# Kernel optimization log

Measured on AMD Instinct MI355X. Metric: run time of the kernel, lower is better.

The kernel has to match this reference:

```python
import jax, jax.numpy as jnp
import numpy as np

EPS = 1e-5

def layernorm(x, g, b):
    mu = jnp.mean(x, axis=-1, keepdims=True)
    var = jnp.mean((x - mu) ** 2, axis=-1, keepdims=True)
    return (x - mu) * jax.lax.rsqrt(var + EPS) * g + b

def cswin_attn(q, k, v, lepe_w, lepe_b, H, W, H_sp, W_sp, num_heads):
    # q,k,v: (B, L, C) with C = branch dim
    B, L, C = q.shape
    d = C // num_heads
    nH, nW = H // H_sp, W // W_sp
    def to_win(t):
        t = t.transpose(0, 2, 1).reshape(B, C, nH, H_sp, nW, W_sp)
        t = t.transpose(0, 2, 4, 3, 5, 1).reshape(B * nH * nW, H_sp * W_sp, num_heads, d)
        return t.transpose(0, 2, 1, 3)  # (Bw, h, N, d)
    kw = to_win(k)
    vw = to_win(v)
    # q windows as images for LePE depthwise conv
    qi = q.transpose(0, 2, 1).reshape(B, C, nH, H_sp, nW, W_sp)
    qi = qi.transpose(0, 2, 4, 1, 3, 5).reshape(B * nH * nW, C, H_sp, W_sp)
    lepe = jax.lax.conv_general_dilated(qi, lepe_w, (1, 1), 'SAME',
                                        feature_group_count=C,
                                        dimension_numbers=('NCHW', 'OIHW', 'NCHW'))
    lepe = lepe + lepe_b[None, :, None, None]
    lepe = lepe.reshape(-1, num_heads, d, H_sp * W_sp).transpose(0, 1, 3, 2)
    qw = qi.reshape(-1, num_heads, d, H_sp * W_sp).transpose(0, 1, 3, 2) * (float(d) ** -0.5)
    attn = jax.nn.softmax(jnp.einsum('whnd,whmd->whnm', qw, kw), axis=-1)
    out = jnp.einsum('whnm,whmd->whnd', attn, vw) + lepe  # (Bw, h, N, d)
    out = out.transpose(0, 2, 1, 3).reshape(B, nH, nW, H_sp, W_sp, C)
    out = out.transpose(0, 1, 3, 2, 4, 5).reshape(B, H * W, C)
    return out

def setup_inputs() -> dict:
    key = jax.random.key(0)
    ks = jax.random.split(key, 20)
    B, C, H, W = 8, 128, 64, 64
    ch_z = 512
    hid = 4 * C
    Cb = C // 2  # branch dim
    s = lambda fin: (1.0 / np.sqrt(fin))
    inp = {
        'x': jax.random.normal(ks[0], (B, C, H, W), jnp.float32),
        'z': jax.random.normal(ks[1], (B, ch_z), jnp.float32),
        'ln1_g': jnp.ones((C,), jnp.float32), 'ln1_b': jnp.zeros((C,), jnp.float32),
        'ln2_g': jnp.ones((C,), jnp.float32), 'ln2_b': jnp.zeros((C,), jnp.float32),
        'Wz1': jax.random.normal(ks[2], (C, ch_z), jnp.float32) * s(ch_z),
        'Wz2': jax.random.normal(ks[3], (C, ch_z), jnp.float32) * s(ch_z),
        'Wqkv': jax.random.normal(ks[4], (3 * C, C), jnp.float32) * s(C),
        'Wproj': jax.random.normal(ks[5], (C, C), jnp.float32) * s(C),
        'bproj': jnp.zeros((C,), jnp.float32),
        'lepe_w0': jax.random.normal(ks[6], (Cb, 1, 3, 3), jnp.float32) * (1.0 / 3.0),
        'lepe_b0': jnp.zeros((Cb,), jnp.float32),
        'lepe_w1': jax.random.normal(ks[7], (Cb, 1, 3, 3), jnp.float32) * (1.0 / 3.0),
        'lepe_b1': jnp.zeros((Cb,), jnp.float32),
        'W1': jax.random.normal(ks[8], (hid, C), jnp.float32) * s(C),
        'b1': jnp.zeros((hid,), jnp.float32),
        'W2': jax.random.normal(ks[9], (C, hid), jnp.float32) * s(hid),
        'b2': jnp.zeros((C,), jnp.float32),
    }
    return inp

def reference(x, z, ln1_g, ln1_b, ln2_g, ln2_b, Wz1, Wz2, Wqkv, Wproj, bproj,
              lepe_w0, lepe_b0, lepe_w1, lepe_b1, W1, b1, W2, b2):
    B, C, H, W = x.shape
    nh = 4  # num_heads // 2 per branch
    ss = 8  # split_size
    Cb = C // 2
    xf = x.reshape(B, C, H * W).transpose(0, 2, 1)  # (B, L, C)
    # code-conditioned attention branch
    z1 = z @ Wz1.T  # (B, C)
    h1 = layernorm(xf, ln1_g, ln1_b) + z1[:, None, :]
    qkv = (h1 @ Wqkv.T).reshape(B, H * W, 3, C).transpose(2, 0, 1, 3)  # (3, B, L, C)
    q, k, v = qkv[0], qkv[1], qkv[2]
    x1 = cswin_attn(q[..., :Cb], k[..., :Cb], v[..., :Cb], lepe_w0, lepe_b0, H, W, H, ss, nh)
    x2 = cswin_attn(q[..., Cb:], k[..., Cb:], v[..., Cb:], lepe_w1, lepe_b1, H, W, ss, W, nh)
    att = jnp.concatenate([x1, x2], axis=2) @ Wproj.T + bproj
    xf = xf + att
    # code-conditioned MLP branch
    z2 = z @ Wz2.T
    h2 = layernorm(xf, ln2_g, ln2_b) + z2[:, None, :]
    mlp = jax.nn.gelu(h2 @ W1.T + b1, approximate=False) @ W2.T + b2
    xf = xf + mlp
    return xf.transpose(0, 2, 1).reshape(B, C, H, W)
```

## Files before the change

kernel.cpp:

```cpp
#include <hip/hip_runtime.h>
#include <cstddef>

__device__ __forceinline__ float b2f(unsigned short u) {
  return __uint_as_float(((unsigned int)u) << 16);
}
__device__ __forceinline__ unsigned short f2b(float f) {
  unsigned int u = __float_as_uint(f);
  u = u + 0x7FFFu + ((u >> 16) & 1u);
  return (unsigned short)(u >> 16);
}
__device__ __forceinline__ unsigned int pk2(float lo, float hi) {
  unsigned int ulo = __float_as_uint(lo) + 0x8000u;
  unsigned int uhi = __float_as_uint(hi) + 0x8000u;
  return __builtin_amdgcn_perm(uhi, ulo, 0x07060302u);
}
__device__ __forceinline__ float gelu_exact(float x) {
  return 0.5f * x * (1.0f + erff(x * 0.70710678118654752f));
}

#if defined(__has_builtin)
#if __has_builtin(__builtin_amdgcn_exp2f)
#define EXP2(x) __builtin_amdgcn_exp2f(x)
#else
#define EXP2(x) __expf((x) * 0.6931471805599453f)
#endif
#else
#define EXP2(x) __expf((x) * 0.6931471805599453f)
#endif

typedef __attribute__((ext_vector_type(8))) short bf16x8;
typedef __attribute__((ext_vector_type(4))) float f32x4;

__global__ void k_detect(const unsigned short* __restrict__ g,
                         unsigned int* __restrict__ flag) {
  if (threadIdx.x == 0 && blockIdx.x == 0) *flag = (g[0] == 0x3F80u) ? 1u : 0u;
}

struct Ptrs18 { const void* p[18]; };
__constant__ const int c_off[19] = {
    0, 4096, 4224, 4352, 4480, 4608, 70144, 135680, 184832, 201216,
    201344, 201920, 201984, 202560, 202624, 268160, 268672, 334208, 334336};

__global__ __launch_bounds__(256) void k_convert(Ptrs18 ptrs,
                                                 const unsigned int* __restrict__ flagp,
                                                 unsigned short* __restrict__ dst) {
  int idx = blockIdx.x * 256 + threadIdx.x;
  if (idx >= 334336) return;
  unsigned int flag = *flagp;
  int i = 0;
#pragma unroll
  for (int t = 1; t < 18; ++t) i += (idx >= c_off[t]);
  int local = idx - c_off[i];
  if (flag) dst[idx] = ((const unsigned short*)ptrs.p[i])[local];
  else      dst[idx] = f2b(((const float*)ptrs.p[i])[local]);
}

__global__ __launch_bounds__(256) void k_transpose_in(const void* __restrict__ x,
                                                      const unsigned int* __restrict__ flagp,
                                                      float* __restrict__ xf) {
  __shared__ float t[32][33];
  unsigned int flag = *flagp;
  int b = blockIdx.z;
  int l0 = blockIdx.x * 32, c0 = blockIdx.y * 32;
  int tx = threadIdx.x & 31, ty = threadIdx.x >> 5;
#pragma unroll
  for (int i = 0; i < 32; i += 8) {
    size_t gi = ((size_t)b * 128 + c0 + ty + i) * 4096 + l0 + tx;
    t[ty + i][tx] = flag ? b2f(((const unsigned short*)x)[gi]) : ((const float*)x)[gi];
  }
  __syncthreads();
#pragma unroll
  for (int i = 0; i < 32; i += 8)
    xf[((size_t)b * 4096 + l0 + ty + i) * 128 + c0 + tx] = t[tx][ty + i];
}

__global__ __launch_bounds__(256) void k_transpose_out(const float* __restrict__ xf,
                                                       const unsigned int* __restrict__ flagp,
                                                       void* __restrict__ out) {
  __shared__ float t[32][33];
  unsigned int flag = *flagp;
  int b = blockIdx.z;
  int l0 = blockIdx.x * 32, c0 = blockIdx.y * 32;
  int tx = threadIdx.x & 31, ty = threadIdx.x >> 5;
#pragma unroll
  for (int i = 0; i < 32; i += 8)
    t[ty + i][tx] = xf[((size_t)b * 4096 + l0 + ty + i) * 128 + c0 + tx];
  __syncthreads();
#pragma unroll
  for (int i = 0; i < 32; i += 8) {
    size_t gi = ((size_t)b * 128 + c0 + ty + i) * 4096 + l0 + tx;
    float v = t[tx][ty + i];
    if (flag) ((unsigned short*)out)[gi] = f2b(v);
    else      ((float*)out)[gi] = v;
  }
}

__global__ __launch_bounds__(256) void k_zmm(const unsigned short* __restrict__ z,
                                             const unsigned short* __restrict__ Wz1,
                                             const unsigned short* __restrict__ Wz2,
                                             float* __restrict__ zz) {
  __shared__ float sz[512];
  int b = blockIdx.x, tid = threadIdx.x;
  sz[tid]       = b2f(z[b * 512 + tid]);
  sz[tid + 256] = b2f(z[b * 512 + 256 + tid]);
  __syncthreads();
  const unsigned short* W = (tid < 128) ? Wz1 : Wz2;
  int c = tid & 127;
  const unsigned short* wr = W + c * 512;
  float acc = 0.f;
  for (int k = 0; k < 512; k += 4) {
    ushort4 wv = *(const ushort4*)&wr[k];
    acc += b2f(wv.x) * sz[k] + b2f(wv.y) * sz[k + 1] + b2f(wv.z) * sz[k + 2] + b2f(wv.w) * sz[k + 3];
  }
  zz[b * 256 + tid] = acc;
}

__global__ __launch_bounds__(256) void k_ln(const float* __restrict__ x,
                                            const unsigned short* __restrict__ g,
                                            const unsigned short* __restrict__ bb,
                                            const float* __restrict__ zz, int zsel,
                                            unsigned short* __restrict__ out) {
  int row = blockIdx.x * 4 + (threadIdx.x >> 6);
  int lane = threadIdx.x & 63;
  int b = row >> 12;
  const float* xr = x + (size_t)row * 128;
  float2 v = *(const float2*)&xr[lane * 2];
  float s = v.x + v.y, s2 = v.x * v.x + v.y * v.y;
#pragma unroll
  for (int m = 32; m; m >>= 1) {
    s += __shfl_xor(s, m, 64);
    s2 += __shfl_xor(s2, m, 64);
  }
  float mu = s * 0.0078125f;
  float var = s2 * 0.0078125f - mu * mu;
  float rstd = rsqrtf(var + 1e-5f);
  int c = lane * 2;
  const float* zr = zz + b * 256 + zsel * 128;
  float ox = (v.x - mu) * rstd * b2f(g[c])     + b2f(bb[c])     + zr[c];
  float oy = (v.y - mu) * rstd * b2f(g[c + 1]) + b2f(bb[c + 1]) + zr[c + 1];
  ushort2 o2; o2.x = f2b(ox); o2.y = f2b(oy);
  *(ushort2*)&out[(size_t)row * 128 + c] = o2;
}

__global__ __launch_bounds__(256) void k_gemm_mfma(const unsigned short* __restrict__ A,
                                                   const unsigned short* __restrict__ W,
                                                   const unsigned short* __restrict__ bias,
                                                   const float* __restrict__ res,
                                                   void* __restrict__ out,
                                                   int M, int N, int K, int ldw, int flags) {
  __shared__ unsigned short As[128][136];
  int bm = blockIdx.x * 128, bn = blockIdx.y * 128;
  int tid = threadIdx.x;
  int lane = tid & 63, wv = tid >> 6;
  int wm = (wv >> 1) * 64, wn = (wv & 1) * 64;
  int qd = lane >> 4, l15 = lane & 15;
#pragma unroll
  for (int i = tid; i < 2048; i += 256) {
    int row = i >> 4, c8 = (i & 15) << 3;
    *(bf16x8*)&As[row][c8] = *(const bf16x8*)&A[(size_t)(bm + row) * 128 + c8];
  }
  __syncthreads();
  f32x4 acc[4][4] = {};
#pragma unroll
  for (int ks = 0; ks < 4; ++ks) {
    bf16x8 af[4], bfr[4];
#pragma unroll
    for (int t = 0; t < 4; ++t) {
      af[t]  = *(const bf16x8*)&As[wm + t * 16 + l15][ks * 32 + qd * 8];
      bfr[t] = *(const bf16x8*)&W[(size_t)(bn + wn + t * 16 + l15) * ldw + ks * 32 + qd * 8];
    }
#pragma unroll
    for (int mi = 0; mi < 4; ++mi)
#pragma unroll
      for (int nj = 0; nj < 4; ++nj)
        acc[mi][nj] = __builtin_amdgcn_mfma_f32_16x16x32_bf16(af[mi], bfr[nj],
                                                              acc[mi][nj], 0, 0, 0);
  }
  if (flags & 4) {
#pragma unroll
    for (int mi = 0; mi < 4; ++mi)
#pragma unroll
      for (int r = 0; r < 4; ++r) {
        int row = bm + wm + mi * 16 + qd * 4 + r;
        int bb2 = row >> 12, l = row & 4095;
        int hI = l >> 6, wI = l & 63;
        int s0 = wI >> 3, t0 = hI * 8 + (wI & 7);
        int s1 = hI >> 3, t1 = (hI & 7) * 64 + wI;
#pragma unroll
        for (int nj = 0; nj < 4; ++nj) {
          int colb = bn + wn + nj * 16;
          int kv = colb >> 7, br = (colb >> 6) & 1, hh2 = (colb >> 4) & 3;
          int ss = br ? s1 : s0, tt = br ? t1 : t0;
          size_t addr = ((((size_t)((kv * 8 + bb2) * 2 + br) * 4 + hh2) * 8 + ss) * 512 + tt) * 16 + l15;
          ((unsigned short*)out)[addr] = f2b(acc[mi][nj][r]);
        }
      }
    return;
  }
  float bv[4];
#pragma unroll
  for (int nj = 0; nj < 4; ++nj)
    bv[nj] = bias ? b2f(bias[bn + wn + nj * 16 + l15]) : 0.f;
#pragma unroll
  for (int mi = 0; mi < 4; ++mi) {
#pragma unroll
    for (int r = 0; r < 4; ++r) {
      int row = bm + wm + mi * 16 + qd * 4 + r;
#pragma unroll
      for (int nj = 0; nj < 4; ++nj) {
        int col = bn + wn + nj * 16 + l15;
        float t = acc[mi][nj][r] + bv[nj];
        if (res) t += res[(size_t)row * N + col];
        if (flags & 2) ((unsigned short*)out)[(size_t)row * N + col] = f2b(t);
        else           ((float*)out)[(size_t)row * N + col] = t;
      }
    }
  }
}

__global__ __launch_bounds__(256) void k_gemm64(const unsigned short* __restrict__ A,
                                                const unsigned short* __restrict__ W,
                                                const unsigned short* __restrict__ bias,
                                                const float* __restrict__ res,
                                                void* __restrict__ out,
                                                int M, int N, int K, int ldw, int flags) {
  __shared__ unsigned short As[64][136];
  int bm = blockIdx.x * 64, bn = blockIdx.y * 128;
  int tid = threadIdx.x;
  int lane = tid & 63, wv = tid >> 6;
  int qd = lane >> 4, l15 = lane & 15;
#pragma unroll
  for (int i = tid; i < 1024; i += 256) {
    int row = i >> 4, c8 = (i & 15) << 3;
    *(bf16x8*)&As[row][c8] = *(const bf16x8*)&A[(size_t)(bm + row) * 128 + c8];
  }
  __syncthreads();
  f32x4 acc[4][2] = {};
#pragma unroll
  for (int ks = 0; ks < 4; ++ks) {
    bf16x8 af[4], bfr[2];
#pragma unroll
    for (int t = 0; t < 4; ++t)
      af[t] = *(const bf16x8*)&As[t * 16 + l15][ks * 32 + qd * 8];
#pragma unroll
    for (int t = 0; t < 2; ++t)
      bfr[t] = *(const bf16x8*)&W[(size_t)(bn + wv * 32 + t * 16 + l15) * ldw + ks * 32 + qd * 8];
#pragma unroll
    for (int mi = 0; mi < 4; ++mi)
#pragma unroll
      for (int nj = 0; nj < 2; ++nj)
        acc[mi][nj] = __builtin_amdgcn_mfma_f32_16x16x32_bf16(af[mi], bfr[nj],
                                                              acc[mi][nj], 0, 0, 0);
  }
  float bv[2];
#pragma unroll
  for (int nj = 0; nj < 2; ++nj)
    bv[nj] = bias ? b2f(bias[bn + wv * 32 + nj * 16 + l15]) : 0.f;
#pragma unroll
  for (int mi = 0; mi < 4; ++mi) {
#pragma unroll
    for (int r = 0; r < 4; ++r) {
      int row = bm + mi * 16 + qd * 4 + r;
#pragma unroll
      for (int nj = 0; nj < 2; ++nj) {
        int col = bn + wv * 32 + nj * 16 + l15;
        float t = acc[mi][nj][r] + bv[nj];
        if (flags & 1) t = gelu_exact(t);
        if (res) t += res[(size_t)row * N + col];
        if (flags & 2) ((unsigned short*)out)[(size_t)row * N + col] = f2b(t);
        else           ((float*)out)[(size_t)row * N + col] = t;
      }
    }
  }
}

__global__ __launch_bounds__(256, 4) void k_mlp(float* __restrict__ xf,
                                                const unsigned short* __restrict__ g,
                                                const unsigned short* __restrict__ bb,
                                                const float* __restrict__ zz,
                                                const unsigned short* __restrict__ W1,
                                                const unsigned short* __restrict__ b1,
                                                const unsigned short* __restrict__ W2,
                                                const unsigned short* __restrict__ b2) {
  __shared__ unsigned short As_all[64][136];
  __shared__ unsigned short Hs[4][64][40];
  int tid = threadIdx.x;
  int bm = blockIdx.x * 64;
  int bidx = bm >> 12;
  {
    int row = tid >> 2, part = tid & 3;
    const float* xr = xf + ((size_t)(bm + row) * 128 + part * 32);
    float v[32];
#pragma unroll
    for (int i = 0; i < 8; ++i) *(float4*)&v[i * 4] = *(const float4*)&xr[i * 4];
    float s = 0.f, s2 = 0.f;
#pragma unroll
    for (int i = 0; i < 32; ++i) { s += v[i]; s2 += v[i] * v[i]; }
    s  += __shfl_xor(s, 1, 64);  s  += __shfl_xor(s, 2, 64);
    s2 += __shfl_xor(s2, 1, 64); s2 += __shfl_xor(s2, 2, 64);
    float mu = s * 0.0078125f;
    float var = s2 * 0.0078125f - mu * mu;
    float rstd = rsqrtf(var + 1e-5f);
    const float* zr = zz + bidx * 256 + 128 + part * 32;
#pragma unroll
    for (int i = 0; i < 32; i += 2) {
      int c = part * 32 + i;
      float ox = (v[i]     - mu) * rstd * b2f(g[c])     + b2f(bb[c])     + zr[i];
      float oy = (v[i + 1] - mu) * rstd * b2f(g[c + 1]) + b2f(bb[c + 1]) + zr[i + 1];
      unsigned int u = (unsigned int)f2b(ox) | ((unsigned int)f2b(oy) << 16);
      *(unsigned int*)&As_all[row][c] = u;
    }
  }
  __syncthreads();
  int lane = tid & 63, wv = tid >> 6;
  int qd = lane >> 4, l15 = lane & 15;
  f32x4 acc2[4][2] = {};
#pragma unroll 1
  for (int j = 0; j < 4; ++j) {
    f32x4 acc1[4][2] = {};
    const unsigned short* W1j = W1 + j * 128 * 128;
#pragma unroll
    for (int ks = 0; ks < 4; ++ks) {
      bf16x8 af[4], bfr[2];
#pragma unroll
      for (int t = 0; t < 4; ++t)
        af[t] = *(const bf16x8*)&As_all[t * 16 + l15][ks * 32 + qd * 8];
#pragma unroll
      for (int t = 0; t < 2; ++t)
        bfr[t] = *(const bf16x8*)&W1j[(wv * 32 + t * 16 + l15) * 128 + ks * 32 + qd * 8];
#pragma unroll
      for (int mi = 0; mi < 4; ++mi)
#pragma unroll
        for (int nj = 0; nj < 2; ++nj)
          acc1[mi][nj] = __builtin_amdgcn_mfma_f32_16x16x32_bf16(af[mi], bfr[nj],
                                                                 acc1[mi][nj], 0, 0, 0);
    }
    if (j) __syncthreads();
    float bv1[2];
#pragma unroll
    for (int nj = 0; nj < 2; ++nj)
      bv1[nj] = b2f(b1[j * 128 + wv * 32 + nj * 16 + l15]);
#pragma unroll
    for (int mi = 0; mi < 4; ++mi)
#pragma unroll
      for (int nj = 0; nj < 2; ++nj)
#pragma unroll
        for (int r = 0; r < 4; ++r) {
          float t = gelu_exact(acc1[mi][nj][r] + bv1[nj]);
          Hs[wv][mi * 16 + qd * 4 + r][nj * 16 + l15] = f2b(t);
        }
    __syncthreads();
#pragma unroll
    for (int ks = 0; ks < 4; ++ks) {
      bf16x8 af2[4], bfr2[2];
#pragma unroll
      for (int t = 0; t < 4; ++t)
        af2[t] = *(const bf16x8*)&Hs[ks][t * 16 + l15][qd * 8];
#pragma unroll
      for (int t = 0; t < 2; ++t)
        bfr2[t] = *(const bf16x8*)&W2[(wv * 32 + t * 16 + l15) * 512 + j * 128 + ks * 32 + qd * 8];
#pragma unroll
      for (int mi = 0; mi < 4; ++mi)
#pragma unroll
        for (int nj = 0; nj < 2; ++nj)
          acc2[mi][nj] = __builtin_amdgcn_mfma_f32_16x16x32_bf16(af2[mi], bfr2[nj],
                                                                 acc2[mi][nj], 0, 0, 0);
    }
  }
  float bv2[2];
#pragma unroll
  for (int nj = 0; nj < 2; ++nj)
    bv2[nj] = b2f(b2[wv * 32 + nj * 16 + l15]);
#pragma unroll
  for (int mi = 0; mi < 4; ++mi)
#pragma unroll
    for (int r = 0; r < 4; ++r) {
      int row = mi * 16 + qd * 4 + r;
#pragma unroll
      for (int nj = 0; nj < 2; ++nj) {
        int col = wv * 32 + nj * 16 + l15;
        size_t gi = (size_t)(bm + row) * 128 + col;
        float t = acc2[mi][nj][r] + bv2[nj] + xf[gi];
        xf[gi] = t;
      }
    }
}

__global__ __launch_bounds__(256, 4) void k_attn_mfma(const unsigned short* __restrict__ qkvw,
                                                      const unsigned short* __restrict__ lw0,
                                                      const unsigned short* __restrict__ lb0,
                                                      const unsigned short* __restrict__ lw1,
                                                      const unsigned short* __restrict__ lb1,
                                                      unsigned short* __restrict__ att) {
  __shared__ unsigned short Ks[512][16];
  __shared__ unsigned short Vt[16][520];
  const size_t S1 = 4194304;
  int branch = blockIdx.y;
  int bx = blockIdx.x;
  int half = bx & 1, wh = bx >> 1;
  int w = wh >> 2, hh = wh & 3;
  int b = w >> 3, s = w & 7;
  int cb = branch * 64 + hh * 16;
  size_t slab = ((size_t)(((b * 2 + branch) * 4 + hh) * 8 + s)) * 8192;
  const unsigned short* Qg = qkvw + slab;
  const unsigned short* Kg = qkvw + S1 + slab;
  const unsigned short* Vg = qkvw + 2 * S1 + slab;
  int tid = threadIdx.x;
  for (int i = tid; i < 1024; i += 256) {
    int tok = i >> 1, c8 = (i & 1) << 3;
    *(bf16x8*)&Ks[tok][c8] = *(const bf16x8*)&Kg[tok * 16 + c8];
    bf16x8 vv = *(const bf16x8*)&Vg[tok * 16 + c8];
    int col = (tok & ~31) | ((tok & 12) << 1) | ((tok & 16) >> 2) | (tok & 3);
#pragma unroll
    for (int j = 0; j < 8; ++j) Vt[c8 + j][col] = (unsigned short)vv[j];
  }
  __syncthreads();
  int lane = tid & 63, wv = tid >> 6;
  int qd = lane >> 4, l15 = lane & 15;
  int koff = (qd & 1) * 8;
  const unsigned short* lwp = branch ? lw1 : lw0;
  const unsigned short* lbp = branch ? lb1 : lb0;
  float wreg[4][9], breg[4];
#pragma unroll
  for (int r = 0; r < 4; ++r) {
    int cc = hh * 16 + qd * 4 + r;
    breg[r] = b2f(lbp[cc]);
#pragma unroll
    for (int j = 0; j < 9; ++j) wreg[r][j] = b2f(lwp[cc * 9 + j]);
  }
  int sy = branch ? 64 : 8;
  int yl = branch ? 8 : 64;
  int xl = branch ? 64 : 8;
  const float QSCALE = 0.25f * 1.44269504f;
  const float NS = -11.5415603f;
  const f32x4 NSHIFT = {NS, NS, NS, NS};
#pragma unroll 1
  for (int qt = 0; qt < 4; ++qt) {
    int q0 = half * 256 + wv * 64 + qt * 16;
    int tq = q0 + l15;
    bf16x8 qf = {};
    if (qd < 2) {
      bf16x8 raw = *(const bf16x8*)&Qg[tq * 16 + qd * 8];
#pragma unroll
      for (int j = 0; j < 8; ++j)
        qf[j] = (short)f2b(b2f((unsigned short)raw[j]) * QSCALE);
    }
    float lsum = 0.f;
    f32x4 O0 = {0.f, 0.f, 0.f, 0.f}, O1 = {0.f, 0.f, 0.f, 0.f};
#pragma unroll 1
    for (int kc = 0; kc < 4; ++kc) {
      f32x4 sc[8];
#pragma unroll
      for (int c = 0; c < 8; ++c) {
        bf16x8 kf = *(const bf16x8*)&Ks[kc * 128 + c * 16 + l15][koff];
        sc[c] = __builtin_amdgcn_mfma_f32_16x16x32_bf16(kf, qf, NSHIFT, 0, 0, 0);
      }
      float csum = 0.f;
#pragma unroll
      for (int c = 0; c < 8; ++c) {
        float e0 = EXP2(sc[c][0]), e1 = EXP2(sc[c][1]);
        float e2 = EXP2(sc[c][2]), e3 = EXP2(sc[c][3]);
        csum += (e0 + e1) + (e2 + e3);
        sc[c][0] = __uint_as_float(pk2(e0, e1));
        sc[c][1] = __uint_as_float(pk2(e2, e3));
      }
      lsum += csum;
#pragma unroll
      for (int bc = 0; bc < 4; ++bc) {
        union { unsigned int u[4]; bf16x8 v; } pu;
        pu.u[0] = __float_as_uint(sc[2 * bc][0]);
        pu.u[1] = __float_as_uint(sc[2 * bc][1]);
        pu.u[2] = __float_as_uint(sc[2 * bc + 1][0]);
        pu.u[3] = __float_as_uint(sc[2 * bc + 1][1]);
        bf16x8 vf = *(const bf16x8*)&Vt[l15][kc * 128 + bc * 32 + qd * 8];
        if (bc & 1) O1 = __builtin_amdgcn_mfma_f32_16x16x32_bf16(vf, pu.v, O1, 0, 0, 0);
        else        O0 = __builtin_amdgcn_mfma_f32_16x16x32_bf16(vf, pu.v, O0, 0, 0, 0);
      }
    }
    lsum += __shfl_xor(lsum, 16, 64);
    lsum += __shfl_xor(lsum, 32, 64);
    int y = branch ? (tq >> 6) : (tq >> 3);
    int x = branch ? (tq & 63) : (tq & 7);
    float lep[4] = {breg[0], breg[1], breg[2], breg[3]};
#pragma unroll
    for (int dy = -1; dy <= 1; ++dy)
#pragma unroll
      for (int dx = -1; dx <= 1; ++dx) {
        if ((unsigned)(y + dy) < (unsigned)yl && (unsigned)(x + dx) < (unsigned)xl) {
          int tn = tq + dy * sy + dx;
          int j = (dy + 1) * 3 + (dx + 1);
          ushort4 qv = *(const ushort4*)&Qg[tn * 16 + qd * 4];
          lep[0] += wreg[0][j] * b2f(qv.x);
          lep[1] += wreg[1][j] * b2f(qv.y);
          lep[2] += wreg[2][j] * b2f(qv.z);
          lep[3] += wreg[3][j] * b2f(qv.w);
        }
      }
    float inv = 1.f / lsum;
    int lo = branch ? (s * 8 + y) * 64 + x : y * 64 + s * 8 + x;
    unsigned short* op = att + ((size_t)(b * 4096 + lo)) * 128 + cb + qd * 4;
    ushort4 o;
    o.x = f2b((O0[0] + O1[0]) * inv + lep[0]);
    o.y = f2b((O0[1] + O1[1]) * inv + lep[1]);
    o.z = f2b((O0[2] + O1[2]) * inv + lep[2]);
    o.w = f2b((O0[3] + O1[3]) * inv + lep[3]);
    *(ushort4*)op = o;
  }
}

extern "C" void kernel_launch(void* const* d_in, const int* in_sizes, int n_in,
                              void* d_out, int out_size, void* d_ws, size_t ws_size,
                              hipStream_t stream) {
  const size_t S = 4194304;
  float* ws = (float*)d_ws;
  unsigned int* flag = (unsigned int*)ws;
  float* zz = ws + 64;
  unsigned short* norm = (unsigned short*)(ws + 2112);
  float* xf = ws + 169472;
  unsigned short* h   = (unsigned short*)(ws + 169472 + S);
  unsigned short* qkv = (unsigned short*)(ws + 169472 + S + S / 2);
  unsigned short* att = h;

  const unsigned short* z     = norm + 0;
  const unsigned short* ln1g  = norm + 4096;
  const unsigned short* ln1b  = norm + 4224;
  const unsigned short* ln2g  = norm + 4352;
  const unsigned short* ln2b  = norm + 4480;
  const unsigned short* Wz1   = norm + 4608;
  const unsigned short* Wz2   = norm + 70144;
  const unsigned short* Wqkv  = norm + 135680;
  const unsigned short* Wproj = norm + 184832;
  const unsigned short* bproj = norm + 201216;
  const unsigned short* lw0   = norm + 201344;
  const unsigned short* lb0   = norm + 201920;
  const unsigned short* lw1   = norm + 201984;
  const unsigned short* lb1   = norm + 202560;
  const unsigned short* W1    = norm + 202624;
  const unsigned short* b1    = norm + 268160;
  const unsigned short* W2    = norm + 268672;
  const unsigned short* b2    = norm + 334208;

  Ptrs18 ptrs;
  for (int i = 0; i < 18; ++i) ptrs.p[i] = d_in[i + 1];

  dim3 t256(256);
  k_detect<<<dim3(1), dim3(64), 0, stream>>>((const unsigned short*)d_in[2], flag);
  k_convert<<<dim3(1306), t256, 0, stream>>>(ptrs, flag, (unsigned short*)norm);
  k_transpose_in<<<dim3(128, 4, 8), t256, 0, stream>>>(d_in[0], flag, xf);
  k_zmm<<<dim3(8), t256, 0, stream>>>(z, Wz1, Wz2, zz);
  k_ln<<<dim3(8192), t256, 0, stream>>>(xf, ln1g, ln1b, zz, 0, h);
  k_gemm_mfma<<<dim3(256, 3), t256, 0, stream>>>(h, Wqkv, nullptr, nullptr, qkv,
                                                 32768, 384, 128, 128, 2 | 4);
  k_attn_mfma<<<dim3(512, 2), t256, 0, stream>>>(qkv, lw0, lb0, lw1, lb1, att);
  k_gemm64<<<dim3(512, 1), t256, 0, stream>>>(att, Wproj, bproj, xf, xf,
                                              32768, 128, 128, 128, 0);
  k_mlp<<<dim3(512), t256, 0, stream>>>(xf, ln2g, ln2b, zz, W1, b1, W2, b2);
  k_transpose_out<<<dim3(128, 4, 8), t256, 0, stream>>>(xf, flag, d_out);
}
```

Measured before the change: 236.5 us.

## Fuse output transpose into MLP, inline dtype detect, MFMA row sums, hw bf16 pack

Drops the separate dtype-detect kernel by having each kernel read the gamma reference directly. Fuses the final NCHW transpose into the MLP kernel's epilogue through a shared-memory tile, so the fp32 residual is no longer written back and re-read. In attention, the softmax row sum is now taken by an extra MFMA against a ones vector, replacing the scalar adds and shuffles. The float-to-bf16 pack now uses the v_cvt_pk_bf16_f32 instruction. This costs one extra MFMA per P·V step, and the sum is now taken over bf16-rounded probabilities.

```diff
diff --git a/kernel.cpp b/kernel.cpp
--- a/kernel.cpp
+++ b/kernel.cpp
@@ -9,10 +9,10 @@
   u = u + 0x7FFFu + ((u >> 16) & 1u);
   return (unsigned short)(u >> 16);
 }
-__device__ __forceinline__ unsigned int pk2(float lo, float hi) {
-  unsigned int ulo = __float_as_uint(lo) + 0x8000u;
-  unsigned int uhi = __float_as_uint(hi) + 0x8000u;
-  return __builtin_amdgcn_perm(uhi, ulo, 0x07060302u);
+__device__ __forceinline__ unsigned int cvtpk(float lo, float hi) {
+  unsigned int r;
+  asm("v_cvt_pk_bf16_f32 %0, %1, %2" : "=v"(r) : "v"(lo), "v"(hi));
+  return r;
 }
 __device__ __forceinline__ float gelu_exact(float x) {
   return 0.5f * x * (1.0f + erff(x * 0.70710678118654752f));
@@ -31,9 +31,8 @@
 typedef __attribute__((ext_vector_type(8))) short bf16x8;
 typedef __attribute__((ext_vector_type(4))) float f32x4;
 
-__global__ void k_detect(const unsigned short* __restrict__ g,
-                         unsigned int* __restrict__ flag) {
-  if (threadIdx.x == 0 && blockIdx.x == 0) *flag = (g[0] == 0x3F80u) ? 1u : 0u;
+__device__ __forceinline__ unsigned int dtype_flag(const unsigned short* gref) {
+  return (gref[0] == 0x3F80u) ? 1u : 0u;
 }
 
 struct Ptrs18 { const void* p[18]; };
@@ -42,11 +41,10 @@
     201344, 201920, 201984, 202560, 202624, 268160, 268672, 334208, 334336};
 
 __global__ __launch_bounds__(256) void k_convert(Ptrs18 ptrs,
-                                                 const unsigned int* __restrict__ flagp,
                                                  unsigned short* __restrict__ dst) {
   int idx = blockIdx.x * 256 + threadIdx.x;
   if (idx >= 334336) return;
-  unsigned int flag = *flagp;
+  unsigned int flag = dtype_flag((const unsigned short*)ptrs.p[1]);
   int i = 0;
 #pragma unroll
   for (int t = 1; t < 18; ++t) i += (idx >= c_off[t]);
@@ -56,10 +54,10 @@
 }
 
 __global__ __launch_bounds__(256) void k_transpose_in(const void* __restrict__ x,
-                                                      const unsigned int* __restrict__ flagp,
+                                                      const unsigned short* __restrict__ gref,
                                                       float* __restrict__ xf) {
   __shared__ float t[32][33];
-  unsigned int flag = *flagp;
+  unsigned int flag = dtype_flag(gref);
   int b = blockIdx.z;
   int l0 = blockIdx.x * 32, c0 = blockIdx.y * 32;
   int tx = threadIdx.x & 31, ty = threadIdx.x >> 5;
@@ -72,27 +70,6 @@
 #pragma unroll
   for (int i = 0; i < 32; i += 8)
     xf[((size_t)b * 4096 + l0 + ty + i) * 128 + c0 + tx] = t[tx][ty + i];
-}
-
-__global__ __launch_bounds__(256) void k_transpose_out(const float* __restrict__ xf,
-                                                       const unsigned int* __restrict__ flagp,
-                                                       void* __restrict__ out) {
-  __shared__ float t[32][33];
-  unsigned int flag = *flagp;
-  int b = blockIdx.z;
-  int l0 = blockIdx.x * 32, c0 = blockIdx.y * 32;
-  int tx = threadIdx.x & 31, ty = threadIdx.x >> 5;
-#pragma unroll
-  for (int i = 0; i < 32; i += 8)
-    t[ty + i][tx] = xf[((size_t)b * 4096 + l0 + ty + i) * 128 + c0 + tx];
-  __syncthreads();
-#pragma unroll
-  for (int i = 0; i < 32; i += 8) {
-    size_t gi = ((size_t)b * 128 + c0 + ty + i) * 4096 + l0 + tx;
-    float v = t[tx][ty + i];
-    if (flag) ((unsigned short*)out)[gi] = f2b(v);
-    else      ((float*)out)[gi] = v;
-  }
 }
 
 __global__ __launch_bounds__(256) void k_zmm(const unsigned short* __restrict__ z,
@@ -274,16 +251,19 @@
   }
 }
 
-__global__ __launch_bounds__(256, 4) void k_mlp(float* __restrict__ xf,
+__global__ __launch_bounds__(256, 4) void k_mlp(const float* __restrict__ xf,
                                                 const unsigned short* __restrict__ g,
                                                 const unsigned short* __restrict__ bb,
                                                 const float* __restrict__ zz,
                                                 const unsigned short* __restrict__ W1,
                                                 const unsigned short* __restrict__ b1,
                                                 const unsigned short* __restrict__ W2,
-                                                const unsigned short* __restrict__ b2) {
-  __shared__ unsigned short As_all[64][136];
-  __shared__ unsigned short Hs[4][64][40];
+                                                const unsigned short* __restrict__ b2,
+                                                const unsigned short* __restrict__ gref,
+                                                void* __restrict__ outp) {
+  __shared__ __align__(16) char smem[37888];
+  unsigned short (*As_all)[136] = (unsigned short(*)[136])smem;
+  unsigned short (*Hs)[64][40]  = (unsigned short(*)[64][40])(smem + 17408);
   int tid = threadIdx.x;
   int bm = blockIdx.x * 64;
   int bidx = bm >> 12;
@@ -371,6 +351,8 @@
 #pragma unroll
   for (int nj = 0; nj < 2; ++nj)
     bv2[nj] = b2f(b2[wv * 32 + nj * 16 + l15]);
+  __syncthreads();
+  float* tile = (float*)smem;
 #pragma unroll
   for (int mi = 0; mi < 4; ++mi)
 #pragma unroll
@@ -380,10 +362,28 @@
       for (int nj = 0; nj < 2; ++nj) {
         int col = wv * 32 + nj * 16 + l15;
         size_t gi = (size_t)(bm + row) * 128 + col;
-        float t = acc2[mi][nj][r] + bv2[nj] + xf[gi];
-        xf[gi] = t;
-      }
-    }
+        tile[col * 68 + row] = acc2[mi][nj][r] + bv2[nj] + xf[gi];
+      }
+    }
+  __syncthreads();
+  unsigned int flag = dtype_flag(gref);
+  int c = tid >> 1, hf = tid & 1;
+  int b = bm >> 12, l0 = (bm & 4095) + hf * 32;
+  const float* tr = &tile[c * 68 + hf * 32];
+  if (flag) {
+    unsigned short* op = (unsigned short*)outp + ((size_t)(b * 128 + c)) * 4096 + l0;
+#pragma unroll
+    for (int i = 0; i < 32; i += 4) {
+      ushort4 o;
+      o.x = f2b(tr[i]); o.y = f2b(tr[i + 1]); o.z = f2b(tr[i + 2]); o.w = f2b(tr[i + 3]);
+      *(ushort4*)&op[i] = o;
+    }
+  } else {
+    float* op = (float*)outp + ((size_t)(b * 128 + c)) * 4096 + l0;
+#pragma unroll
+    for (int i = 0; i < 32; i += 4)
+      *(float4*)&op[i] = *(const float4*)&tr[i];
+  }
 }
 
 __global__ __launch_bounds__(256, 4) void k_attn_mfma(const unsigned short* __restrict__ qkvw,
@@ -428,6 +428,9 @@
 #pragma unroll
     for (int j = 0; j < 9; ++j) wreg[r][j] = b2f(lwp[cc * 9 + j]);
   }
+  bf16x8 onesv;
+#pragma unroll
+  for (int j = 0; j < 8; ++j) onesv[j] = (short)0x3F80;
   int sy = branch ? 64 : 8;
   int yl = branch ? 8 : 64;
   int xl = branch ? 64 : 8;
@@ -445,8 +448,8 @@
       for (int j = 0; j < 8; ++j)
         qf[j] = (short)f2b(b2f((unsigned short)raw[j]) * QSCALE);
     }
-    float lsum = 0.f;
     f32x4 O0 = {0.f, 0.f, 0.f, 0.f}, O1 = {0.f, 0.f, 0.f, 0.f};
+    f32x4 Osum = {0.f, 0.f, 0.f, 0.f};
 #pragma unroll 1
     for (int kc = 0; kc < 4; ++kc) {
       f32x4 sc[8];
@@ -455,16 +458,13 @@
         bf16x8 kf = *(const bf16x8*)&Ks[kc * 128 + c * 16 + l15][koff];
         sc[c] = __builtin_amdgcn_mfma_f32_16x16x32_bf16(kf, qf, NSHIFT, 0, 0, 0);
       }
-      float csum = 0.f;
 #pragma unroll
       for (int c = 0; c < 8; ++c) {
         float e0 = EXP2(sc[c][0]), e1 = EXP2(sc[c][1]);
         float e2 = EXP2(sc[c][2]), e3 = EXP2(sc[c][3]);
-        csum += (e0 + e1) + (e2 + e3);
-        sc[c][0] = __uint_as_float(pk2(e0, e1));
-        sc[c][1] = __uint_as_float(pk2(e2, e3));
-      }
-      lsum += csum;
+        sc[c][0] = __uint_as_float(cvtpk(e0, e1));
+        sc[c][1] = __uint_as_float(cvtpk(e2, e3));
+      }
 #pragma unroll
       for (int bc = 0; bc < 4; ++bc) {
         union { unsigned int u[4]; bf16x8 v; } pu;
@@ -473,12 +473,11 @@
         pu.u[2] = __float_as_uint(sc[2 * bc + 1][0]);
         pu.u[3] = __float_as_uint(sc[2 * bc + 1][1]);
         bf16x8 vf = *(const bf16x8*)&Vt[l15][kc * 128 + bc * 32 + qd * 8];
+        Osum = __builtin_amdgcn_mfma_f32_16x16x32_bf16(onesv, pu.v, Osum, 0, 0, 0);
         if (bc & 1) O1 = __builtin_amdgcn_mfma_f32_16x16x32_bf16(vf, pu.v, O1, 0, 0, 0);
         else        O0 = __builtin_amdgcn_mfma_f32_16x16x32_bf16(vf, pu.v, O0, 0, 0, 0);
       }
     }
-    lsum += __shfl_xor(lsum, 16, 64);
-    lsum += __shfl_xor(lsum, 32, 64);
     int y = branch ? (tq >> 6) : (tq >> 3);
     int x = branch ? (tq & 63) : (tq & 7);
     float lep[4] = {breg[0], breg[1], breg[2], breg[3]};
@@ -496,7 +495,7 @@
           lep[3] += wreg[3][j] * b2f(qv.w);
         }
       }
-    float inv = 1.f / lsum;
+    float inv = 1.f / Osum[0];
     int lo = branch ? (s * 8 + y) * 64 + x : y * 64 + s * 8 + x;
     unsigned short* op = att + ((size_t)(b * 4096 + lo)) * 128 + cb + qd * 4;
     ushort4 o;
@@ -513,7 +512,6 @@
                               hipStream_t stream) {
   const size_t S = 4194304;
   float* ws = (float*)d_ws;
-  unsigned int* flag = (unsigned int*)ws;
   float* zz = ws + 64;
   unsigned short* norm = (unsigned short*)(ws + 2112);
   float* xf = ws + 169472;
@@ -540,13 +538,14 @@
   const unsigned short* W2    = norm + 268672;
   const unsigned short* b2    = norm + 334208;
 
+  const unsigned short* gref = (const unsigned short*)d_in[2];
+
   Ptrs18 ptrs;
   for (int i = 0; i < 18; ++i) ptrs.p[i] = d_in[i + 1];
 
   dim3 t256(256);
-  k_detect<<<dim3(1), dim3(64), 0, stream>>>((const unsigned short*)d_in[2], flag);
-  k_convert<<<dim3(1306), t256, 0, stream>>>(ptrs, flag, (unsigned short*)norm);
-  k_transpose_in<<<dim3(128, 4, 8), t256, 0, stream>>>(d_in[0], flag, xf);
+  k_convert<<<dim3(1306), t256, 0, stream>>>(ptrs, (unsigned short*)norm);
+  k_transpose_in<<<dim3(128, 4, 8), t256, 0, stream>>>(d_in[0], gref, xf);
   k_zmm<<<dim3(8), t256, 0, stream>>>(z, Wz1, Wz2, zz);
   k_ln<<<dim3(8192), t256, 0, stream>>>(xf, ln1g, ln1b, zz, 0, h);
   k_gemm_mfma<<<dim3(256, 3), t256, 0, stream>>>(h, Wqkv, nullptr, nullptr, qkv,
@@ -554,6 +553,6 @@
   k_attn_mfma<<<dim3(512, 2), t256, 0, stream>>>(qkv, lw0, lb0, lw1, lb1, att);
   k_gemm64<<<dim3(512, 1), t256, 0, stream>>>(att, Wproj, bproj, xf, xf,
                                               32768, 128, 128, 128, 0);
-  k_mlp<<<dim3(512), t256, 0, stream>>>(xf, ln2g, ln2b, zz, W1, b1, W2, b2);
-  k_transpose_out<<<dim3(128, 4, 8), t256, 0, stream>>>(xf, flag, d_out);
-}
+  k_mlp<<<dim3(512), t256, 0, stream>>>(xf, ln2g, ln2b, zz, W1, b1, W2, b2,
+                                        gref, d_out);
+}
```

Measured after the change: 228.6 us. -3.3%, faster.
